# Optimization experiments

Measured on AMD Instinct MI355X. Metric: run time of the kernel, lower is better.

Reference implementation:

```python
import jax, jax.numpy as jnp
import numpy as np

NUM_HEADS = 16
THETA = 10000.0


def _rope(x, pos, theta):
    # x: [b, h, s, d_k] with d_k even; rotate interleaved pairs (even, odd)
    d = x.shape[-1]
    inv_freq = theta ** (-jnp.arange(0, d, 2, dtype=jnp.float32) / d)  # [d/2]
    ang = pos.astype(jnp.float32)[:, None] * inv_freq                  # [s, d/2]
    cos = jnp.cos(ang)[None, None]                                     # [1,1,s,d/2]
    sin = jnp.sin(ang)[None, None]
    x1 = x[..., 0::2]
    x2 = x[..., 1::2]
    r1 = x1 * cos - x2 * sin
    r2 = x1 * sin + x2 * cos
    return jnp.stack([r1, r2], axis=-1).reshape(x.shape)


def setup_inputs() -> dict:
    key = jax.random.key(0)
    ks = jax.random.split(key, 5)
    B, S, D = 2, 2048, 1024
    x = jax.random.normal(ks[0], (B, S, D), dtype=jnp.float32)
    scale = 0.02
    Wq = jax.random.normal(ks[1], (D, D), dtype=jnp.float32) * scale
    Wk = jax.random.normal(ks[2], (D, D), dtype=jnp.float32) * scale
    Wv = jax.random.normal(ks[3], (D, D), dtype=jnp.float32) * scale
    Wo = jax.random.normal(ks[4], (D, D), dtype=jnp.float32) * scale
    return {"x": x, "Wq": Wq, "Wk": Wk, "Wv": Wv, "Wo": Wo}


def reference(x, Wq, Wk, Wv, Wo):
    B, S, D = x.shape
    H = NUM_HEADS
    dk = D // H
    # QKV projections (bias-free Linear: y = x @ W^T, W is [out, in])
    q = (x @ Wq.T).reshape(B, S, H, dk).transpose(0, 2, 1, 3)  # [b,h,s,dk]
    k = (x @ Wk.T).reshape(B, S, H, dk).transpose(0, 2, 1, 3)
    v = (x @ Wv.T).reshape(B, S, H, dk).transpose(0, 2, 1, 3)
    pos = jnp.arange(S)
    q = _rope(q, pos, THETA)
    k = _rope(k, pos, THETA)
    # naive masked SDPA, causal mask
    scores = jnp.einsum('bhqd,bhkd->bhqk', q, k) / (dk ** 0.5)
    causal = jnp.tril(jnp.ones((S, S), dtype=bool))
    scores = jnp.where(causal, scores, -jnp.inf)
    attn = jax.nn.softmax(scores, axis=-1)
    out = jnp.einsum('bhqk,bhkd->bhqd', attn, v)
    out = out.transpose(0, 2, 1, 3).reshape(B, S, D)
    return out @ Wo.T
```

## Files before the change

kernel.cpp:

```cpp
#include <hip/hip_runtime.h>
#include <hip/hip_bf16.h>
#include <stdint.h>

typedef __bf16 bf16;
typedef __bf16 bf16x8 __attribute__((ext_vector_type(8)));
typedef float f32x4 __attribute__((ext_vector_type(4)));
typedef float f32x16 __attribute__((ext_vector_type(16)));

#define B_ 2
#define S_ 2048
#define D_ 1024
#define H_ 16
#define DK 64
#define M_ 4096

__device__ __forceinline__ void gload_lds16(const void* g, void* l) {
  __builtin_amdgcn_global_load_lds(
      (const __attribute__((address_space(1))) uint32_t*)(uintptr_t)g,
      (__attribute__((address_space(3))) uint32_t*)(uintptr_t)l, 16, 0, 0);
}

__device__ __forceinline__ uint32_t pkbf(float a, float b) {
  union { uint32_t u; struct { bf16 x, y; } s; } r;
  r.s.x = (bf16)a; r.s.y = (bf16)b;
  return r.u;
}

struct alignas(8) B4s { bf16 a, b, c, d; };

__global__ __launch_bounds__(256) void cvt_all_kernel(
    const float* __restrict__ x, const float* __restrict__ wq, const float* __restrict__ wk,
    const float* __restrict__ wv, const float* __restrict__ wo,
    bf16* __restrict__ xb, bf16* __restrict__ wqb, bf16* __restrict__ wkb,
    bf16* __restrict__ wvb, bf16* __restrict__ wob) {
  int i = blockIdx.x * 256 + threadIdx.x;
  const float* src;
  bf16* dst;
  int off;
  if (i < 1048576) { src = x; dst = xb; off = i; }
  else if (i < 1310720) { src = wq; dst = wqb; off = i - 1048576; }
  else if (i < 1572864) { src = wk; dst = wkb; off = i - 1310720; }
  else if (i < 1835008) { src = wv; dst = wvb; off = i - 1572864; }
  else { src = wo; dst = wob; off = i - 1835008; }
  float4 v = reinterpret_cast<const float4*>(src)[off];
  B4s o{(bf16)v.x, (bf16)v.y, (bf16)v.z, (bf16)v.w};
  reinterpret_cast<B4s*>(dst)[off] = o;
}

template <int MODE>
__global__ __launch_bounds__(256, 3) void gemm_kernel(
    const bf16* __restrict__ A,
    const bf16* __restrict__ W0, const bf16* __restrict__ W1, const bf16* __restrict__ W2,
    bf16* __restrict__ q_out, bf16* __restrict__ k_out, bf16* __restrict__ v_out,
    float* __restrict__ c_out) {
  constexpr int BK = 64;
  constexpr int BM = (MODE == 0) ? 128 : 64;
  constexpr int AM = (MODE == 0) ? 2 : 1;
  constexpr int NT = (MODE == 0) ? 24 : 8;
  constexpr int PERX = (MODE == 0) ? 96 : 64;
  __shared__ bf16 Alds[BM * BK];
  __shared__ bf16 Blds[128 * BK];
  const int tid = threadIdx.x;
  const int w = tid >> 6, l = tid & 63;
  const int l31 = l & 31, hh = l >> 5;
  const int lin = (blockIdx.x & 7) * PERX + (blockIdx.x >> 3);
  const int m0 = (lin / NT) * BM;
  const int nt = lin % NT;
  const bf16* W;
  int n0;
  const int rt = (MODE == 0) ? (nt >> 3) : 0;
  if (MODE == 0) {
    W = rt == 0 ? W0 : (rt == 1 ? W1 : W2);
    n0 = (nt & 7) * 128;
  } else {
    W = W0;
    n0 = nt * 128;
  }
  const int K = 1024;
  const int wm = (MODE == 0) ? (w >> 1) * 64 : (w & 1) * 32;
  const int wn = (MODE == 0) ? (w & 1) * 64 : (w >> 1) * 64;
  const int srow = w * 8 + (l >> 3);
  const int scol = ((l & 7) * 8) ^ (((l >> 3) & 7) * 8);
  const int swz = (l & 7) * 8;
  f32x16 acc[AM][2] = {};
  for (int k0 = 0; k0 < K; k0 += BK) {
    const bf16* Ab = A + (size_t)m0 * K + k0;
    const bf16* Bb = W + (size_t)n0 * K + k0;
#pragma unroll
    for (int c = 0; c < BM / 32; ++c)
      gload_lds16(Ab + (size_t)(c * 32 + srow) * K + scol, Alds + (c * 32 + w * 8) * BK);
#pragma unroll
    for (int c = 0; c < 4; ++c)
      gload_lds16(Bb + (size_t)(c * 32 + srow) * K + scol, Blds + (c * 32 + w * 8) * BK);
    __syncthreads();
    bf16x8 af[AM][4], bfr[2][4];
#pragma unroll
    for (int am = 0; am < AM; ++am)
#pragma unroll
      for (int t = 0; t < 4; ++t)
        af[am][t] = *reinterpret_cast<const bf16x8*>(
            Alds + (wm + am * 32 + l31) * BK + ((t * 16 + hh * 8) ^ swz));
#pragma unroll
    for (int bn = 0; bn < 2; ++bn)
#pragma unroll
      for (int t = 0; t < 4; ++t)
        bfr[bn][t] = *reinterpret_cast<const bf16x8*>(
            Blds + (wn + bn * 32 + l31) * BK + ((t * 16 + hh * 8) ^ swz));
#pragma unroll
    for (int t = 0; t < 4; ++t)
#pragma unroll
      for (int am = 0; am < AM; ++am)
#pragma unroll
        for (int bn = 0; bn < 2; ++bn)
          acc[am][bn] = __builtin_amdgcn_mfma_f32_32x32x16_bf16(af[am][t], bfr[bn][t],
                                                               acc[am][bn], 0, 0, 0);
    __syncthreads();
  }
#pragma unroll
  for (int am = 0; am < AM; ++am)
#pragma unroll
    for (int bn = 0; bn < 2; ++bn)
#pragma unroll
      for (int r = 0; r < 16; ++r) {
        int m = m0 + wm + am * 32 + (r & 3) + 8 * (r >> 2) + 4 * hh;
        int n = n0 + wn + bn * 32 + l31;
        float v = acc[am][bn][r];
        if (MODE == 0) {
          bf16* dst = rt == 0 ? q_out : (rt == 1 ? k_out : v_out);
          int h = n >> 6, d = n & 63;
          int b = m >> 11, s = m & 2047;
          dst[(((size_t)b * H_ + h) * S_ + s) * DK + d] = (bf16)v;
        } else {
          c_out[(size_t)m * D_ + n] = v;
        }
      }
}

__global__ __launch_bounds__(256) void rope_kernel(bf16* __restrict__ Q, bf16* __restrict__ K) {
  const int NG = 32 * 2048 * 8;
  int idx = blockIdx.x * 256 + threadIdx.x;
  bf16* X = Q;
  float sc = 0.18033688f;
  if (idx >= NG) { X = K; idx -= NG; sc = 1.0f; }
  int g = idx & 7;
  int s = (idx >> 3) & 2047;
  int bh = idx >> 14;
  size_t off = ((size_t)bh * S_ + s) * DK + g * 8;
  bf16x8 v = *reinterpret_cast<const bf16x8*>(X + off);
  bf16x8 o;
  const float c0 = -0.4152410118609203f;
  float fs = (float)s;
#pragma unroll
  for (int p = 0; p < 4; ++p) {
    int i = g * 4 + p;
    float ang = fs * exp2f((float)i * c0);
    float sn = __sinf(ang), cs = __cosf(ang);
    float x1 = (float)v[2 * p], x2 = (float)v[2 * p + 1];
    o[2 * p]     = (bf16)((x1 * cs - x2 * sn) * sc);
    o[2 * p + 1] = (bf16)((x1 * sn + x2 * cs) * sc);
  }
  *reinterpret_cast<bf16x8*>(X + off) = o;
}

__global__ __launch_bounds__(256, 4) void attn_kernel(
    const bf16* __restrict__ Q, const bf16* __restrict__ K, const bf16* __restrict__ V,
    bf16* __restrict__ O) {
  __shared__ __align__(16) char smem[40960];
  bf16* K3 = (bf16*)smem;
  bf16* Vt2 = (bf16*)smem + 12288;
  float* MG = (float*)smem;
  const int tid = threadIdx.x;
  const int w = tid >> 6, l = tid & 63;
  const int ql = l & 31, h = l >> 5;
  const int kh = w >> 1, qh = w & 1;
  const int qt = 31 - (int)(blockIdx.x >> 5);
  const int bh = blockIdx.x & 31;
  const size_t base = (size_t)bh * S_ * DK;

  const size_t qrow = base + (size_t)(qt * 64 + qh * 32 + ql) * DK;
  bf16x8 qf[4];
#pragma unroll
  for (int t = 0; t < 4; ++t)
    qf[t] = *reinterpret_cast<const bf16x8*>(Q + qrow + t * 16 + h * 8);

  float l_run = 0.f;
  f32x16 o0 = {}, o1 = {};

  auto stageK = [&](int kt, int buf) {
#pragma unroll
    for (int c = 0; c < 2; ++c) {
      int row = c * 32 + w * 8 + (l >> 3);
      int col = ((l & 7) * 8) ^ ((row & 7) * 8);
      gload_lds16(K + base + (size_t)(kt * 64 + row) * DK + col,
                  K3 + buf * 4096 + c * 2048 + w * 512);
    }
  };
  auto loadV = [&](int kt, bf16x8 (&pv)[2]) {
    const bf16* vp = V + base + (size_t)(kt * 64 + l) * DK + w * 16;
    pv[0] = *reinterpret_cast<const bf16x8*>(vp);
    pv[1] = *reinterpret_cast<const bf16x8*>(vp + 8);
  };
  auto writeV = [&](int vb, const bf16x8 (&pv)[2]) {
    bf16* Vt = Vt2 + vb * 4096;
#pragma unroll
    for (int j = 0; j < 8; ++j) {
      Vt[(w * 16 + j) * 64 + (l ^ (j * 8))] = pv[0][j];
      Vt[(w * 16 + 8 + j) * 64 + (l ^ (j * 8))] = pv[1][j];
    }
  };

  {
    bf16x8 pv[2];
    loadV(0, pv);
    stageK(0, 0);
    if (qt >= 1) stageK(1, 1);
    writeV(0, pv);
    if (qt >= 1) {
      asm volatile("s_waitcnt vmcnt(2)" ::: "memory");
    } else {
      asm volatile("s_waitcnt vmcnt(0)" ::: "memory");
    }
    asm volatile("s_waitcnt lgkmcnt(0)" ::: "memory");
    __builtin_amdgcn_sched_barrier(0);
    __builtin_amdgcn_s_barrier();
    __builtin_amdgcn_sched_barrier(0);
  }

  const int swzd = (ql & 7) * 8;
  const int keyA = kh * 32 + ql;
  const int limq = qh * 32 + ql;
  bf16x8 pvv[2];
  int kb = 0, kb2 = 2;

  for (int kt = 0; kt <= qt; ++kt) {
    const int vb = kt & 1;
    const bool pre = kt < qt;
    const bool pre2 = kt + 2 <= qt;
    const bool lastt = (kt == qt);
    const bool skipw = lastt && (kh == 1) && (qh == 0);
    if (pre) loadV(kt + 1, pvv);
    if (pre2) stageK(kt + 2, kb2);
    if (!skipw) {
      f32x16 ss = {};
      __builtin_amdgcn_s_setprio(1);
#pragma unroll
      for (int t = 0; t < 4; ++t) {
        bf16x8 kf = *reinterpret_cast<const bf16x8*>(
            K3 + kb * 4096 + keyA * 64 + ((t * 16 + h * 8) ^ ((keyA & 7) * 8)));
        ss = __builtin_amdgcn_mfma_f32_32x32x16_bf16(kf, qf[t], ss, 0, 0, 0);
      }
      __builtin_amdgcn_s_setprio(0);
      if (lastt) {
#pragma unroll
        for (int r = 0; r < 16; ++r) {
          int kl = kh * 32 + (r & 3) + 8 * (r >> 2) + 4 * h;
          if (kl > limq) ss[r] = -INFINITY;
        }
      }
      float t0 = 0.f, t1 = 0.f, t2 = 0.f, t3 = 0.f;
#pragma unroll
      for (int r = 0; r < 16; r += 4) {
        float p0 = exp2f(ss[r]);
        float p1 = exp2f(ss[r + 1]);
        float p2 = exp2f(ss[r + 2]);
        float p3 = exp2f(ss[r + 3]);
        ss[r] = p0; ss[r + 1] = p1; ss[r + 2] = p2; ss[r + 3] = p3;
        t0 += p0; t1 += p1; t2 += p2; t3 += p3;
      }
      l_run += (t0 + t1) + (t2 + t3);
      uint32_t Wq_[4][2];
#pragma unroll
      for (int g = 0; g < 4; ++g) {
        Wq_[g][0] = pkbf(ss[4 * g + 0], ss[4 * g + 1]);
        Wq_[g][1] = pkbf(ss[4 * g + 2], ss[4 * g + 3]);
      }
      __builtin_amdgcn_s_setprio(1);
#pragma unroll
      for (int ks = 0; ks < 2; ++ks) {
        uint32_t a0 = Wq_[2 * ks][0], a1 = Wq_[2 * ks][1];
        uint32_t b0 = Wq_[2 * ks + 1][0], b1 = Wq_[2 * ks + 1][1];
        uint32_t sxa0 = (uint32_t)__shfl_xor((int)a0, 32);
        uint32_t sxa1 = (uint32_t)__shfl_xor((int)a1, 32);
        uint32_t sxb0 = (uint32_t)__shfl_xor((int)b0, 32);
        uint32_t sxb1 = (uint32_t)__shfl_xor((int)b1, 32);
        union { uint32_t u[4]; bf16x8 v; } pa;
        pa.u[0] = h ? sxb0 : a0;
        pa.u[1] = h ? sxb1 : a1;
        pa.u[2] = h ? b0 : sxa0;
        pa.u[3] = h ? b1 : sxa1;
        int col = (kh * 32 + ks * 16 + h * 8) ^ swzd;
        const bf16* Vt = Vt2 + vb * 4096;
        bf16x8 v0 = *reinterpret_cast<const bf16x8*>(&Vt[ql * 64 + col]);
        bf16x8 v1 = *reinterpret_cast<const bf16x8*>(&Vt[(32 + ql) * 64 + col]);
        o0 = __builtin_amdgcn_mfma_f32_32x32x16_bf16(pa.v, v0, o0, 0, 0, 0);
        o1 = __builtin_amdgcn_mfma_f32_32x32x16_bf16(pa.v, v1, o1, 0, 0, 0);
      }
      __builtin_amdgcn_s_setprio(0);
    }
    if (pre) writeV(vb ^ 1, pvv);
    asm volatile("s_waitcnt vmcnt(2)" ::: "memory");
    asm volatile("s_waitcnt lgkmcnt(0)" ::: "memory");
    __builtin_amdgcn_sched_barrier(0);
    __builtin_amdgcn_s_barrier();
    __builtin_amdgcn_sched_barrier(0);
    kb = (kb == 2) ? 0 : kb + 1;
    kb2 = (kb2 == 2) ? 0 : kb2 + 1;
  }

  l_run += __shfl_xor(l_run, 32);
  __syncthreads();
  if (kh == 1) {
    int off = (qh * 64 + l) * 33;
    MG[off] = l_run;
#pragma unroll
    for (int r = 0; r < 16; ++r) {
      MG[off + 1 + r] = o0[r];
      MG[off + 17 + r] = o1[r];
    }
  }
  __syncthreads();
  if (kh == 0) {
    int off = (qh * 64 + l) * 33;
    float inv = 1.0f / (l_run + MG[off]);
    const int b = bh >> 4, hd = bh & 15;
#pragma unroll
    for (int r = 0; r < 16; ++r) {
      int rowl = (r & 3) + 8 * (r >> 2) + 4 * h;
      float invr = __shfl(inv, rowl);
      int qr = qt * 64 + qh * 32 + rowl;
      size_t ooff = ((size_t)b * S_ + qr) * D_ + hd * 64;
      O[ooff + ql] = (bf16)((o0[r] + MG[off + 1 + r]) * invr);
      O[ooff + 32 + ql] = (bf16)((o1[r] + MG[off + 17 + r]) * invr);
    }
  }
}

extern "C" void kernel_launch(void* const* d_in, const int* in_sizes, int n_in,
                              void* d_out, int out_size, void* d_ws, size_t ws_size,
                              hipStream_t stream) {
  const float* x  = (const float*)d_in[0];
  const float* Wq = (const float*)d_in[1];
  const float* Wk = (const float*)d_in[2];
  const float* Wv = (const float*)d_in[3];
  const float* Wo = (const float*)d_in[4];
  float* out = (float*)d_out;
  char* ws = (char*)d_ws;

  bf16* xb  = (bf16*)(ws + ((size_t)0 << 20));
  bf16* wqb = (bf16*)(ws + ((size_t)8 << 20));
  bf16* wkb = (bf16*)(ws + ((size_t)10 << 20));
  bf16* wvb = (bf16*)(ws + ((size_t)12 << 20));
  bf16* wob = (bf16*)(ws + ((size_t)14 << 20));
  bf16* Qb  = (bf16*)(ws + ((size_t)16 << 20));
  bf16* Kb  = (bf16*)(ws + ((size_t)24 << 20));
  bf16* Vb  = (bf16*)(ws + ((size_t)32 << 20));
  bf16* Ob  = (bf16*)(ws + ((size_t)40 << 20));

  cvt_all_kernel<<<8192, 256, 0, stream>>>(x, Wq, Wk, Wv, Wo, xb, wqb, wkb, wvb, wob);
  gemm_kernel<0><<<768, 256, 0, stream>>>(xb, wqb, wkb, wvb, Qb, Kb, Vb, nullptr);
  rope_kernel<<<4096, 256, 0, stream>>>(Qb, Kb);
  attn_kernel<<<1024, 256, 0, stream>>>(Qb, Kb, Vb, Ob);
  gemm_kernel<1><<<512, 256, 0, stream>>>(Ob, wob, nullptr, nullptr, nullptr, nullptr,
                                          nullptr, out);
}
```

Before: 107.9 us.

## Fuse Q RoPE into attention Q load and remap attention block schedule

The Q rotary embedding and softmax scale now happen when the attention kernel loads its Q fragments, so the separate RoPE pass only touches K and launches half as many blocks. This removes one read and one write of the Q tensor. The attention block index mapping also changes: odd blocks take query tiles in ascending order and even blocks in descending order, and heads are interleaved, to even out causal work across concurrently running blocks. The cost is extra sin/cos/exp2 arithmetic at the start of each attention block.

Measured after the change: 116.5 us. 1.08x slower.

```diff
diff --git a/kernel.cpp b/kernel.cpp
--- a/kernel.cpp
+++ b/kernel.cpp
@@ -136,17 +136,13 @@
       }
 }
 
-__global__ __launch_bounds__(256) void rope_kernel(bf16* __restrict__ Q, bf16* __restrict__ K) {
-  const int NG = 32 * 2048 * 8;
+__global__ __launch_bounds__(256) void rope_kernel(bf16* __restrict__ K) {
   int idx = blockIdx.x * 256 + threadIdx.x;
-  bf16* X = Q;
-  float sc = 0.18033688f;
-  if (idx >= NG) { X = K; idx -= NG; sc = 1.0f; }
   int g = idx & 7;
   int s = (idx >> 3) & 2047;
   int bh = idx >> 14;
   size_t off = ((size_t)bh * S_ + s) * DK + g * 8;
-  bf16x8 v = *reinterpret_cast<const bf16x8*>(X + off);
+  bf16x8 v = *reinterpret_cast<const bf16x8*>(K + off);
   bf16x8 o;
   const float c0 = -0.4152410118609203f;
   float fs = (float)s;
@@ -156,10 +152,10 @@
     float ang = fs * exp2f((float)i * c0);
     float sn = __sinf(ang), cs = __cosf(ang);
     float x1 = (float)v[2 * p], x2 = (float)v[2 * p + 1];
-    o[2 * p]     = (bf16)((x1 * cs - x2 * sn) * sc);
-    o[2 * p + 1] = (bf16)((x1 * sn + x2 * cs) * sc);
-  }
-  *reinterpret_cast<bf16x8*>(X + off) = o;
+    o[2 * p]     = (bf16)(x1 * cs - x2 * sn);
+    o[2 * p + 1] = (bf16)(x1 * sn + x2 * cs);
+  }
+  *reinterpret_cast<bf16x8*>(K + off) = o;
 }
 
 __global__ __launch_bounds__(256, 4) void attn_kernel(
@@ -173,15 +169,34 @@
   const int w = tid >> 6, l = tid & 63;
   const int ql = l & 31, h = l >> 5;
   const int kh = w >> 1, qh = w & 1;
-  const int qt = 31 - (int)(blockIdx.x >> 5);
-  const int bh = blockIdx.x & 31;
+  const int bid = blockIdx.x;
+  const int qt = (bid & 1) ? (bid >> 5) : 31 - (bid >> 5);
+  const int bh = (bid & 3) * 8 + ((bid >> 2) & 7);
   const size_t base = (size_t)bh * S_ * DK;
 
-  const size_t qrow = base + (size_t)(qt * 64 + qh * 32 + ql) * DK;
+  const int qs = qt * 64 + qh * 32 + ql;
+  const size_t qrow = base + (size_t)qs * DK;
   bf16x8 qf[4];
-#pragma unroll
-  for (int t = 0; t < 4; ++t)
-    qf[t] = *reinterpret_cast<const bf16x8*>(Q + qrow + t * 16 + h * 8);
+  {
+    const float c0 = -0.4152410118609203f;
+    const float qsc = 0.18033688f;
+    const float fs = (float)qs;
+#pragma unroll
+    for (int t = 0; t < 4; ++t) {
+      bf16x8 raw = *reinterpret_cast<const bf16x8*>(Q + qrow + t * 16 + h * 8);
+      bf16x8 rq;
+#pragma unroll
+      for (int p = 0; p < 4; ++p) {
+        int i = t * 8 + h * 4 + p;
+        float ang = fs * exp2f((float)i * c0);
+        float sn = __sinf(ang), cs = __cosf(ang);
+        float x1 = (float)raw[2 * p], x2 = (float)raw[2 * p + 1];
+        rq[2 * p]     = (bf16)((x1 * cs - x2 * sn) * qsc);
+        rq[2 * p + 1] = (bf16)((x1 * sn + x2 * cs) * qsc);
+      }
+      qf[t] = rq;
+    }
+  }
 
   float l_run = 0.f;
   f32x16 o0 = {}, o1 = {};
@@ -358,7 +373,7 @@
 
   cvt_all_kernel<<<8192, 256, 0, stream>>>(x, Wq, Wk, Wv, Wo, xb, wqb, wkb, wvb, wob);
   gemm_kernel<0><<<768, 256, 0, stream>>>(xb, wqb, wkb, wvb, Qb, Kb, Vb, nullptr);
-  rope_kernel<<<4096, 256, 0, stream>>>(Qb, Kb);
+  rope_kernel<<<2048, 256, 0, stream>>>(Kb);
   attn_kernel<<<1024, 256, 0, stream>>>(Qb, Kb, Vb, Ob);
   gemm_kernel<1><<<512, 256, 0, stream>>>(Ob, wob, nullptr, nullptr, nullptr, nullptr,
                                           nullptr, out);
```
